# Kernel optimization log

Measured on AMD Instinct MI355X. Metric: run time of the kernel, lower is better.

The kernel has to match this reference:

```python
import jax, jax.numpy as jnp
import numpy as np

IN_SZ = 256
OUT_SZ = 256
RANK = 60  # min(60, IN_SZ*OUT_SZ)
C = 512    # channel_size
N_SEL = 256
B = 1024


def setup_inputs() -> dict:
    key = jax.random.key(0)
    k_x, k_u, k_v, k_b, k_i = jax.random.split(key, 5)
    # match torch init scales: U ~ U(-sqrt(3/rank), ...), V ~ U(-sqrt(1/(in*out)),...)
    bu = np.sqrt(3.0 / RANK)
    bv = np.sqrt(1.0 / (IN_SZ * OUT_SZ))
    bb = np.sqrt(1.0 / RANK)
    x = jax.random.normal(k_x, (N_SEL, B, IN_SZ), dtype=jnp.float32)
    weights_U = jax.random.uniform(k_u, (C, RANK), jnp.float32, -bu, bu)
    weights_V = jax.random.uniform(k_v, (RANK, IN_SZ * OUT_SZ), jnp.float32, -bv, bv)
    bias = jax.random.uniform(k_b, (C, 1, OUT_SZ), jnp.float32, -bb, bb)
    indices = jax.random.randint(k_i, (N_SEL,), 0, C, dtype=jnp.int64)
    return {"x": x, "indices": indices, "weights_U": weights_U,
            "weights_V": weights_V, "bias": bias}


def reference(x, indices, weights_U, weights_V, bias):
    # Synthesize full per-channel weights, then gather selected channels
    # (faithful to the original: full U @ V materialized before gather).
    weight = (weights_U @ weights_V).reshape(-1, IN_SZ, OUT_SZ)  # [C, in, out]
    w = weight[indices]                                          # [n, in, out]
    # per-channel batched matmul: [n, B, in] x [n, in, out] -> [n, B, out]
    out = jnp.einsum('nbi,nio->nbo', x, w) + bias[indices]
    return out
```

## Files before the change

### kernel.cpp

```cpp
#include <hip/hip_runtime.h>
#include <hip/hip_bf16.h>
#include <stdint.h>

#define IN_SZ   256
#define OUT_SZ  256
#define RANK    60
#define NSEL    256
#define BATCH   1024
#define WELEMS  (IN_SZ * OUT_SZ)

typedef __attribute__((ext_vector_type(8))) short          short8;
typedef __attribute__((ext_vector_type(4))) float          f32x4;
typedef __attribute__((ext_vector_type(4))) unsigned short u16x4;

static __device__ __forceinline__ unsigned short f32_to_bf16(float f) {
    union { float f; uint32_t u; } c; c.f = f;
    uint32_t u = c.u;
    u += 0x7fffu + ((u >> 16) & 1u);
    return (unsigned short)(u >> 16);
}

__global__ __launch_bounds__(256) void synth_w(
    const float* __restrict__ U, const float* __restrict__ V,
    const int* __restrict__ idx, unsigned short* __restrict__ wt)
{
    __shared__ unsigned short Cs[16][2064];

    int bid = blockIdx.x;
    int L   = (bid & 7) * 64 + (bid >> 3);
    int ic  = L >> 4;
    int g16 = L & 15;

    int tid = threadIdx.x, lane = tid & 63, wv = tid >> 6;

    int arow = lane & 15;
    int c    = idx[g16 * 16 + arow];
    short8 afr[2];
    #pragma unroll
    for (int ks = 0; ks < 2; ++ks) {
        short8 h;
        #pragma unroll
        for (int j = 0; j < 8; ++j) {
            int r = ks * 32 + (lane >> 4) * 8 + j;
            float u = (r < RANK) ? U[c * RANK + r] : 0.f;
            h[j] = (short)f32_to_bf16(u);
        }
        afr[ks] = h;
    }

    const float* Vb = V + (size_t)ic * 2048;
    #pragma unroll 2
    for (int mt = 0; mt < 32; ++mt) {
        int mloc = (wv * 32 + mt) * 16 + (lane & 15);
        f32x4 acc = {};
        #pragma unroll
        for (int ks = 0; ks < 2; ++ks) {
            short8 b;
            #pragma unroll
            for (int j = 0; j < 8; ++j) {
                int r = ks * 32 + (lane >> 4) * 8 + j;
                float v = (r < RANK) ? Vb[(size_t)r * WELEMS + mloc] : 0.f;
                b[j] = (short)f32_to_bf16(v);
            }
            acc = __builtin_amdgcn_mfma_f32_16x16x32_bf16(afr[ks], b, acc, 0, 0, 0);
        }
        #pragma unroll
        for (int j = 0; j < 4; ++j) {
            int nl = (lane >> 4) * 4 + j;
            Cs[nl][wv * 512 + mt * 16 + (lane & 15)] = f32_to_bf16(acc[j]);
        }
    }
    __syncthreads();

    #pragma unroll
    for (int t0 = 0; t0 < 16; ++t0) {
        int t  = t0 * 256 + tid;
        int nl = t >> 8;
        int o  = t & 255;
        short8 h;
        #pragma unroll
        for (int il = 0; il < 8; ++il) h[il] = (short)Cs[nl][il * 256 + o];
        int n = g16 * 16 + nl;
        size_t base = (size_t)n * WELEMS + (size_t)ic * 2048 + (size_t)((o ^ (ic & 3)) * 8);
        *reinterpret_cast<short8*>(wt + base) = h;
    }
}

__global__ __launch_bounds__(256) void gemm_k(
    const float* __restrict__ x, const int* __restrict__ idx,
    const unsigned short* __restrict__ wt, const float* __restrict__ bias,
    float* __restrict__ out)
{
    __shared__ __align__(16) unsigned short As[2][64 * 64];
    __shared__ __align__(16) unsigned short Bs[2][8 * 256 * 8];

    int bid = blockIdx.x;
    int L   = (bid & 7) * 512 + (bid >> 3);
    int n   = L >> 4;
    int mt  = L & 15;

    int tid  = threadIdx.x;
    int lane = tid & 63;
    int wv   = tid >> 6;

    const float*          xn = x  + (size_t)n * (BATCH * IN_SZ) + (size_t)mt * 64 * IN_SZ;
    const unsigned short* wn = wt + (size_t)n * WELEMS;

    f32x4 acc[4][4] = {};

    auto stageA_load = [&](int kt, float4* va) {
        #pragma unroll
        for (int p = 0; p < 4; ++p) {
            int id  = tid + p * 256;
            int row = id >> 4, c4 = id & 15;
            va[p] = *reinterpret_cast<const float4*>(
                xn + (size_t)row * IN_SZ + kt * 64 + c4 * 4);
        }
    };
    auto stageA_write = [&](int buf, const float4* va) {
        #pragma unroll
        for (int p = 0; p < 4; ++p) {
            int id  = tid + p * 256;
            int row = id >> 4, c4 = id & 15;
            u16x4 h;
            h[0] = f32_to_bf16(va[p].x); h[1] = f32_to_bf16(va[p].y);
            h[2] = f32_to_bf16(va[p].z); h[3] = f32_to_bf16(va[p].w);
            int off = row * 128 + ((c4 * 8) ^ ((row & 7) << 4));
            *reinterpret_cast<u16x4*>(&As[buf][off >> 1]) = h;
        }
    };
    auto stageB = [&](int buf, int kt) {
        #pragma unroll
        for (int p = 0; p < 8; ++p) {
            int seg = wv * 8 + p;
            const unsigned short* gp = wn + (size_t)kt * 16384 + (size_t)seg * 512 + lane * 8;
            __builtin_amdgcn_global_load_lds(
                (const __attribute__((address_space(1))) void*)gp,
                (__attribute__((address_space(3))) void*)(&Bs[buf][seg * 512]),
                16, 0, 0);
        }
    };
    auto compute = [&](int buf) {
        #pragma unroll
        for (int kk = 0; kk < 2; ++kk) {
            short8 af[4], bf[4];
            int krow = kk * 32 + (lane >> 4) * 8;
            #pragma unroll
            for (int mf = 0; mf < 4; ++mf) {
                int row = mf * 16 + (lane & 15);
                int off = row * 128 + ((krow * 2) ^ ((row & 7) << 4));
                af[mf] = *reinterpret_cast<const short8*>(&As[buf][off >> 1]);
            }
            int gi = kk * 4 + (lane >> 4);
            #pragma unroll
            for (int nf = 0; nf < 4; ++nf) {
                int o   = wv * 64 + nf * 16 + (lane & 15);
                int off = gi * 4096 + ((o ^ (gi & 3)) * 16);
                bf[nf] = *reinterpret_cast<const short8*>(&Bs[buf][off >> 1]);
            }
            #pragma unroll
            for (int mf = 0; mf < 4; ++mf)
                #pragma unroll
                for (int nf = 0; nf < 4; ++nf)
                    acc[mf][nf] = __builtin_amdgcn_mfma_f32_16x16x32_bf16(
                        af[mf], bf[nf], acc[mf][nf], 0, 0, 0);
        }
    };

    {
        float4 va[4];
        stageA_load(0, va);
        stageB(0, 0);
        stageA_write(0, va);
    }
    __syncthreads();

    int cur = 0;
    #pragma unroll
    for (int kt = 0; kt < 4; ++kt) {
        float4 va[4];
        if (kt < 3) {
            stageA_load(kt + 1, va);
            stageB(cur ^ 1, kt + 1);
        }
        compute(cur);
        if (kt < 3) stageA_write(cur ^ 1, va);
        __syncthreads();
        cur ^= 1;
    }

    int c = idx[n];
    float bv[4];
    #pragma unroll
    for (int nf = 0; nf < 4; ++nf)
        bv[nf] = bias[(size_t)c * OUT_SZ + wv * 64 + nf * 16 + (lane & 15)];

    float* on = out + (size_t)n * (BATCH * OUT_SZ) + (size_t)mt * 64 * OUT_SZ;
    #pragma unroll
    for (int mf = 0; mf < 4; ++mf) {
        int r0 = mf * 16 + (lane >> 4) * 4;
        #pragma unroll
        for (int nf = 0; nf < 4; ++nf) {
            int o = wv * 64 + nf * 16 + (lane & 15);
            #pragma unroll
            for (int j = 0; j < 4; ++j)
                on[(size_t)(r0 + j) * OUT_SZ + o] = acc[mf][nf][j] + bv[nf];
        }
    }
}

extern "C" void kernel_launch(void* const* d_in, const int* in_sizes, int n_in,
                              void* d_out, int out_size, void* d_ws, size_t ws_size,
                              hipStream_t stream) {
    const float* x    = (const float*)d_in[0];
    const int*   idx  = (const int*)  d_in[1];
    const float* U    = (const float*)d_in[2];
    const float* V    = (const float*)d_in[3];
    const float* bias = (const float*)d_in[4];
    float* out = (float*)d_out;
    unsigned short* wt = (unsigned short*)d_ws;
    (void)in_sizes; (void)n_in; (void)out_size; (void)ws_size;

    synth_w<<<dim3(512),  dim3(256), 0, stream>>>(U, V, idx, wt);
    gemm_k <<<dim3(4096), dim3(256), 0, stream>>>(x, idx, wt, bias, out);
}
```

Baseline: 182.2 us.

## Load whole A tile once into LDS and read B fragments directly from global

The gemm kernel now loads the full 64x256 x tile, converted to bf16, into LDS in a single pass. It drops the double-buffered K pipeline and the LDS staging of the weight matrix; weight fragments are read straight from global/L2 memory into registers. The weight layout XOR swizzle is removed to match, and launch bounds request 3 blocks per CU. This cuts barriers and LDS traffic and raises occupancy. In exchange it loses the load/compute overlap and relies on cache hits for the repeated B reads across the 16 M-tiles of each channel.

```diff
diff --git a/kernel.cpp b/kernel.cpp
--- a/kernel.cpp
+++ b/kernel.cpp
@@ -81,18 +81,17 @@
         #pragma unroll
         for (int il = 0; il < 8; ++il) h[il] = (short)Cs[nl][il * 256 + o];
         int n = g16 * 16 + nl;
-        size_t base = (size_t)n * WELEMS + (size_t)ic * 2048 + (size_t)((o ^ (ic & 3)) * 8);
+        size_t base = (size_t)n * WELEMS + (size_t)ic * 2048 + (size_t)o * 8;
         *reinterpret_cast<short8*>(wt + base) = h;
     }
 }
 
-__global__ __launch_bounds__(256) void gemm_k(
+__global__ __launch_bounds__(256, 3) void gemm_k(
     const float* __restrict__ x, const int* __restrict__ idx,
     const unsigned short* __restrict__ wt, const float* __restrict__ bias,
     float* __restrict__ out)
 {
-    __shared__ __align__(16) unsigned short As[2][64 * 64];
-    __shared__ __align__(16) unsigned short Bs[2][8 * 256 * 8];
+    __shared__ __align__(16) unsigned short As[64 * 256];
 
     int bid = blockIdx.x;
     int L   = (bid & 7) * 512 + (bid >> 3);
@@ -102,106 +101,68 @@
     int tid  = threadIdx.x;
     int lane = tid & 63;
     int wv   = tid >> 6;
+    int r16  = lane & 15;
+    int q    = lane >> 4;
 
     const float*          xn = x  + (size_t)n * (BATCH * IN_SZ) + (size_t)mt * 64 * IN_SZ;
-    const unsigned short* wn = wt + (size_t)n * WELEMS;
+    const unsigned short* wb = wt + (size_t)n * WELEMS;
+
+    #pragma unroll
+    for (int p = 0; p < 8; ++p) {
+        int id    = p * 256 + tid;
+        int row   = id >> 5;
+        int chunk = id & 31;
+        const float* gp = xn + (size_t)row * IN_SZ + chunk * 8;
+        float4 v0 = *reinterpret_cast<const float4*>(gp);
+        float4 v1 = *reinterpret_cast<const float4*>(gp + 4);
+        short8 h;
+        h[0] = (short)f32_to_bf16(v0.x); h[1] = (short)f32_to_bf16(v0.y);
+        h[2] = (short)f32_to_bf16(v0.z); h[3] = (short)f32_to_bf16(v0.w);
+        h[4] = (short)f32_to_bf16(v1.x); h[5] = (short)f32_to_bf16(v1.y);
+        h[6] = (short)f32_to_bf16(v1.z); h[7] = (short)f32_to_bf16(v1.w);
+        int off = row * 512 + ((chunk * 16) ^ ((row & 7) << 4));
+        *reinterpret_cast<short8*>(&As[off >> 1]) = h;
+    }
+    __syncthreads();
 
     f32x4 acc[4][4] = {};
 
-    auto stageA_load = [&](int kt, float4* va) {
+    #pragma unroll
+    for (int ks = 0; ks < 8; ++ks) {
+        short8 af[4], bf[4];
         #pragma unroll
-        for (int p = 0; p < 4; ++p) {
-            int id  = tid + p * 256;
-            int row = id >> 4, c4 = id & 15;
-            va[p] = *reinterpret_cast<const float4*>(
-                xn + (size_t)row * IN_SZ + kt * 64 + c4 * 4);
+        for (int mf = 0; mf < 4; ++mf) {
+            int row = mf * 16 + r16;
+            int off = row * 512 + ((ks * 64 + q * 16) ^ ((row & 7) << 4));
+            af[mf] = *reinterpret_cast<const short8*>(&As[off >> 1]);
         }
-    };
-    auto stageA_write = [&](int buf, const float4* va) {
         #pragma unroll
-        for (int p = 0; p < 4; ++p) {
-            int id  = tid + p * 256;
-            int row = id >> 4, c4 = id & 15;
-            u16x4 h;
-            h[0] = f32_to_bf16(va[p].x); h[1] = f32_to_bf16(va[p].y);
-            h[2] = f32_to_bf16(va[p].z); h[3] = f32_to_bf16(va[p].w);
-            int off = row * 128 + ((c4 * 8) ^ ((row & 7) << 4));
-            *reinterpret_cast<u16x4*>(&As[buf][off >> 1]) = h;
+        for (int nf = 0; nf < 4; ++nf) {
+            int o = wv * 64 + nf * 16 + r16;
+            bf[nf] = *reinterpret_cast<const short8*>(
+                wb + (size_t)((ks * 4 + q) * 2048 + o * 8));
         }
-    };
-    auto stageB = [&](int buf, int kt) {
         #pragma unroll
-        for (int p = 0; p < 8; ++p) {
-            int seg = wv * 8 + p;
-            const unsigned short* gp = wn + (size_t)kt * 16384 + (size_t)seg * 512 + lane * 8;
-            __builtin_amdgcn_global_load_lds(
-                (const __attribute__((address_space(1))) void*)gp,
-                (__attribute__((address_space(3))) void*)(&Bs[buf][seg * 512]),
-                16, 0, 0);
-        }
-    };
-    auto compute = [&](int buf) {
-        #pragma unroll
-        for (int kk = 0; kk < 2; ++kk) {
-            short8 af[4], bf[4];
-            int krow = kk * 32 + (lane >> 4) * 8;
+        for (int mf = 0; mf < 4; ++mf)
             #pragma unroll
-            for (int mf = 0; mf < 4; ++mf) {
-                int row = mf * 16 + (lane & 15);
-                int off = row * 128 + ((krow * 2) ^ ((row & 7) << 4));
-                af[mf] = *reinterpret_cast<const short8*>(&As[buf][off >> 1]);
-            }
-            int gi = kk * 4 + (lane >> 4);
-            #pragma unroll
-            for (int nf = 0; nf < 4; ++nf) {
-                int o   = wv * 64 + nf * 16 + (lane & 15);
-                int off = gi * 4096 + ((o ^ (gi & 3)) * 16);
-                bf[nf] = *reinterpret_cast<const short8*>(&Bs[buf][off >> 1]);
-            }
-            #pragma unroll
-            for (int mf = 0; mf < 4; ++mf)
-                #pragma unroll
-                for (int nf = 0; nf < 4; ++nf)
-                    acc[mf][nf] = __builtin_amdgcn_mfma_f32_16x16x32_bf16(
-                        af[mf], bf[nf], acc[mf][nf], 0, 0, 0);
-        }
-    };
-
-    {
-        float4 va[4];
-        stageA_load(0, va);
-        stageB(0, 0);
-        stageA_write(0, va);
-    }
-    __syncthreads();
-
-    int cur = 0;
-    #pragma unroll
-    for (int kt = 0; kt < 4; ++kt) {
-        float4 va[4];
-        if (kt < 3) {
-            stageA_load(kt + 1, va);
-            stageB(cur ^ 1, kt + 1);
-        }
-        compute(cur);
-        if (kt < 3) stageA_write(cur ^ 1, va);
-        __syncthreads();
-        cur ^= 1;
+            for (int nf = 0; nf < 4; ++nf)
+                acc[mf][nf] = __builtin_amdgcn_mfma_f32_16x16x32_bf16(
+                    af[mf], bf[nf], acc[mf][nf], 0, 0, 0);
     }
 
     int c = idx[n];
     float bv[4];
     #pragma unroll
     for (int nf = 0; nf < 4; ++nf)
-        bv[nf] = bias[(size_t)c * OUT_SZ + wv * 64 + nf * 16 + (lane & 15)];
+        bv[nf] = bias[(size_t)c * OUT_SZ + wv * 64 + nf * 16 + r16];
 
     float* on = out + (size_t)n * (BATCH * OUT_SZ) + (size_t)mt * 64 * OUT_SZ;
     #pragma unroll
     for (int mf = 0; mf < 4; ++mf) {
-        int r0 = mf * 16 + (lane >> 4) * 4;
+        int r0 = mf * 16 + q * 4;
         #pragma unroll
         for (int nf = 0; nf < 4; ++nf) {
-            int o = wv * 64 + nf * 16 + (lane & 15);
+            int o = wv * 64 + nf * 16 + r16;
             #pragma unroll
             for (int j = 0; j < 4; ++j)
                 on[(size_t)(r0 + j) * OUT_SZ + o] = acc[mf][nf][j] + bv[nf];
```

Result: faster. 171.4 us (-5.9%).
